# Optimization experiments

Measured on AMD Instinct MI355X. Metric: run time of the kernel, lower is better.

Reference implementation:

```python
import jax, jax.numpy as jnp
import numpy as np

D_MODEL = 1024
N_HEADS = 16
HEAD_DIM = D_MODEL // N_HEADS


def setup_inputs() -> dict:
    key = jax.random.key(0)
    ks = jax.random.split(key, 9)
    s = 1.0 / np.sqrt(D_MODEL)
    x = jax.random.normal(ks[0], (1, 4096, D_MODEL), dtype=jnp.float32)
    Wq = jax.random.uniform(ks[1], (D_MODEL, D_MODEL), jnp.float32, -s, s)
    bq = jax.random.uniform(ks[2], (D_MODEL,), jnp.float32, -s, s)
    Wk = jax.random.uniform(ks[3], (D_MODEL, D_MODEL), jnp.float32, -s, s)
    bk = jax.random.uniform(ks[4], (D_MODEL,), jnp.float32, -s, s)
    Wv = jax.random.uniform(ks[5], (D_MODEL, D_MODEL), jnp.float32, -s, s)
    bv = jax.random.uniform(ks[6], (D_MODEL,), jnp.float32, -s, s)
    Wo = jax.random.uniform(ks[7], (D_MODEL, D_MODEL), jnp.float32, -s, s)
    bo = jax.random.uniform(ks[8], (D_MODEL,), jnp.float32, -s, s)
    return {"x": x, "Wq": Wq, "bq": bq, "Wk": Wk, "bk": bk,
            "Wv": Wv, "bv": bv, "Wo": Wo, "bo": bo, "layer_id": 0}


def reference(x, Wq, bq, Wk, bk, Wv, bv, Wo, bo, layer_id):
    # Fresh-cache path: K/V projected from x, then cached (cache omitted here).
    B, T, C = x.shape
    H, Dh = N_HEADS, HEAD_DIM

    def proj(W, b):
        # nn.Linear: x @ W.T + b, then split heads -> [B, H, T, Dh]
        y = jnp.einsum('btc,dc->btd', x, W) + b
        return y.reshape(B, T, H, Dh).transpose(0, 2, 1, 3)

    q = proj(Wq, bq)
    k = proj(Wk, bk)
    v = proj(Wv, bv)

    scores = jnp.einsum('bhqd,bhkd->bhqk', q, k) * (Dh ** -0.5)
    attn = jax.nn.softmax(scores, axis=-1)
    out = jnp.einsum('bhqk,bhkd->bhqd', attn, v)  # [B,H,T,Dh]
    out = out.transpose(0, 2, 1, 3).reshape(B, T, C)
    return jnp.einsum('btc,dc->btd', out, Wo) + bo
```

## Files before the change

kernel.cpp:

```cpp
#include <hip/hip_runtime.h>
#include <stdint.h>
#include <math.h>

#define T_SEQ 4096
#define DM 1024
#define NH 16
#define DH 64
#define QSCALE 0.1803368801111137f

typedef unsigned short u16;
typedef __attribute__((ext_vector_type(8))) short bfx8;
typedef __attribute__((ext_vector_type(4))) float f4;
typedef __attribute__((ext_vector_type(16))) float f16f;
typedef __attribute__((ext_vector_type(4))) uint32_t u32x4;

__device__ inline u16 f2bf(float f) {
  uint32_t u = __float_as_uint(f);
  u = (u + 0x7fffu + ((u >> 16) & 1u)) >> 16;
  return (u16)u;
}

__device__ inline uint32_t cvtpk(float lo, float hi) {
  uint32_t r;
  asm("v_cvt_pk_bf16_f32 %0, %1, %2" : "=v"(r) : "v"(lo), "v"(hi));
  return r;
}
__device__ inline void pl32(uint32_t &a, uint32_t &b) {
  asm volatile("v_permlane32_swap_b32 %0, %1" : "+v"(a), "+v"(b));
}

__device__ inline void gl_lds16(const void* g, void* l) {
  __builtin_amdgcn_global_load_lds(
      (__attribute__((address_space(1))) uint32_t*)const_cast<void*>(g),
      (__attribute__((address_space(3))) uint32_t*)l, 16, 0, 0);
}

__global__ __launch_bounds__(256) void cvt_kernel(const float* __restrict__ src,
                                                  u16* __restrict__ dst, int n8) {
  int i = blockIdx.x * 256 + threadIdx.x;
  if (i >= n8) return;
  const float4* s = (const float4*)src + (size_t)i * 2;
  float4 a = s[0], b = s[1];
  union { u16 u[8]; bfx8 v; } o;
  o.u[0] = f2bf(a.x); o.u[1] = f2bf(a.y); o.u[2] = f2bf(a.z); o.u[3] = f2bf(a.w);
  o.u[4] = f2bf(b.x); o.u[5] = f2bf(b.y); o.u[6] = f2bf(b.z); o.u[7] = f2bf(b.w);
  *(bfx8*)(dst + (size_t)i * 8) = o.v;
}

__global__ __launch_bounds__(256) void cvt4_kernel(
    const float* __restrict__ a, const float* __restrict__ b,
    const float* __restrict__ c, const float* __restrict__ d,
    u16* __restrict__ oa, u16* __restrict__ ob, u16* __restrict__ oc, u16* __restrict__ od) {
  int z = blockIdx.y;
  const float* s = (z == 0) ? a : (z == 1) ? b : (z == 2) ? c : d;
  u16* o = (z == 0) ? oa : (z == 1) ? ob : (z == 2) ? oc : od;
  int i = blockIdx.x * 256 + threadIdx.x;
  const float4* sp = (const float4*)s + (size_t)i * 2;
  float4 x = sp[0], y = sp[1];
  union { u16 u[8]; bfx8 v; } t;
  t.u[0] = f2bf(x.x); t.u[1] = f2bf(x.y); t.u[2] = f2bf(x.z); t.u[3] = f2bf(x.w);
  t.u[4] = f2bf(y.x); t.u[5] = f2bf(y.y); t.u[6] = f2bf(y.z); t.u[7] = f2bf(y.w);
  *(bfx8*)(o + (size_t)i * 8) = t.v;
}

__global__ __launch_bounds__(256) void gemm_qkv(
    const u16* __restrict__ xb,
    const u16* __restrict__ wq, const u16* __restrict__ wk, const u16* __restrict__ wv,
    const float* __restrict__ bq, const float* __restrict__ bk, const float* __restrict__ bv,
    u16* __restrict__ qo, u16* __restrict__ ko, u16* __restrict__ vo) {
  __shared__ u16 sA[128 * 32];
  __shared__ u16 sB[128 * 32];
  const int mode = blockIdx.z;
  const u16* w = (mode == 0) ? wq : (mode == 1) ? wk : wv;
  const float* bias = (mode == 0) ? bq : (mode == 1) ? bk : bv;
  const int tid = threadIdx.x, lane = tid & 63, wid = tid >> 6;
  const int wr = wid >> 1, wc = wid & 1;
  const int row0 = blockIdx.y * 128, col0 = blockIdx.x * 128;
  f4 acc[4][4] = {};

  for (int kt = 0; kt < DM / 32; ++kt) {
#pragma unroll
    for (int i = 0; i < 2; ++i) {
      int c = i * 4 + wid;
      int r = c * 16 + (lane >> 2);
      int s = (lane & 3) ^ ((r >> 1) & 3);
      gl_lds16(xb + (size_t)(row0 + r) * DM + kt * 32 + s * 8, &sA[c * 512 + lane * 8]);
      gl_lds16(w  + (size_t)(col0 + r) * DM + kt * 32 + s * 8, &sB[c * 512 + lane * 8]);
    }
    __syncthreads();
    bfx8 a[4], b[4];
#pragma unroll
    for (int t = 0; t < 4; ++t) {
      int ra = wr * 64 + t * 16 + (lane & 15);
      a[t] = *(const bfx8*)&sA[ra * 32 + (((lane >> 4) ^ ((ra >> 1) & 3)) * 8)];
      int rb = wc * 64 + t * 16 + (lane & 15);
      b[t] = *(const bfx8*)&sB[rb * 32 + (((lane >> 4) ^ ((rb >> 1) & 3)) * 8)];
    }
#pragma unroll
    for (int mt = 0; mt < 4; ++mt)
#pragma unroll
      for (int nt = 0; nt < 4; ++nt)
        acc[mt][nt] = __builtin_amdgcn_mfma_f32_16x16x32_bf16(a[mt], b[nt], acc[mt][nt], 0, 0, 0);
    __syncthreads();
  }

#pragma unroll
  for (int mt = 0; mt < 4; ++mt) {
#pragma unroll
    for (int nt = 0; nt < 4; ++nt) {
      int n = col0 + wc * 64 + nt * 16 + (lane & 15);
      float bv_ = bias[n];
      int h = n >> 6, d = n & 63;
#pragma unroll
      for (int r = 0; r < 4; ++r) {
        int mrow = row0 + wr * 64 + mt * 16 + (lane >> 4) * 4 + r;
        float v = acc[mt][nt][r] + bv_;
        if (mode == 0)      qo[(size_t)h * (T_SEQ * DH) + (size_t)mrow * DH + d] = f2bf(v * QSCALE);
        else if (mode == 1) ko[(size_t)h * (T_SEQ * DH) + (size_t)mrow * DH + d] = f2bf(v);
        else                vo[(size_t)h * (DH * T_SEQ) + (size_t)d * T_SEQ + mrow] = f2bf(v);
      }
    }
  }
}

__global__ __launch_bounds__(256) void gemm_out(
    const u16* __restrict__ ab, const u16* __restrict__ wo,
    const float* __restrict__ bo, float* __restrict__ out) {
  __shared__ u16 sA[128 * 32];
  __shared__ u16 sB[128 * 32];
  const int tid = threadIdx.x, lane = tid & 63, wid = tid >> 6;
  const int wr = wid >> 1, wc = wid & 1;
  const int row0 = blockIdx.y * 128, col0 = blockIdx.x * 128;
  f4 acc[4][4] = {};

  for (int kt = 0; kt < DM / 32; ++kt) {
#pragma unroll
    for (int i = 0; i < 2; ++i) {
      int c = i * 4 + wid;
      int r = c * 16 + (lane >> 2);
      int s = (lane & 3) ^ ((r >> 1) & 3);
      gl_lds16(ab + (size_t)(row0 + r) * DM + kt * 32 + s * 8, &sA[c * 512 + lane * 8]);
      gl_lds16(wo + (size_t)(col0 + r) * DM + kt * 32 + s * 8, &sB[c * 512 + lane * 8]);
    }
    __syncthreads();
    bfx8 a[4], b[4];
#pragma unroll
    for (int t = 0; t < 4; ++t) {
      int ra = wr * 64 + t * 16 + (lane & 15);
      a[t] = *(const bfx8*)&sA[ra * 32 + (((lane >> 4) ^ ((ra >> 1) & 3)) * 8)];
      int rb = wc * 64 + t * 16 + (lane & 15);
      b[t] = *(const bfx8*)&sB[rb * 32 + (((lane >> 4) ^ ((rb >> 1) & 3)) * 8)];
    }
#pragma unroll
    for (int mt = 0; mt < 4; ++mt)
#pragma unroll
      for (int nt = 0; nt < 4; ++nt)
        acc[mt][nt] = __builtin_amdgcn_mfma_f32_16x16x32_bf16(a[mt], b[nt], acc[mt][nt], 0, 0, 0);
    __syncthreads();
  }

#pragma unroll
  for (int mt = 0; mt < 4; ++mt) {
#pragma unroll
    for (int nt = 0; nt < 4; ++nt) {
      int n = col0 + wc * 64 + nt * 16 + (lane & 15);
      float bv_ = bo[n];
#pragma unroll
      for (int r = 0; r < 4; ++r) {
        int mrow = row0 + wr * 64 + mt * 16 + (lane >> 4) * 4 + r;
        out[(size_t)mrow * DM + n] = acc[mt][nt][r] + bv_;
      }
    }
  }
}

__global__ __launch_bounds__(512, 2) void attn_kernel(
    const u16* __restrict__ qb, const u16* __restrict__ kb,
    const u16* __restrict__ vb, u16* __restrict__ ao) {
  __shared__ u16 sK[2][64 * 64];
  __shared__ u16 sV[2][64 * 64];
  const int tid = threadIdx.x, lane = tid & 63, wid = tid >> 6;
  const int hi = lane >> 5, q32 = lane & 31;
  const int bid = blockIdx.x;
  const int h = (bid & 7) * 2 + ((bid >> 3) & 1);
  const int qr0 = (bid >> 4) * 256 + wid * 32;
  const size_t hoff = (size_t)h * ((size_t)T_SEQ * DH);

  bfx8 qf0, qf1, qf2, qf3;
  {
    const u16* qp = qb + hoff + (size_t)(qr0 + q32) * DH + hi * 8;
    qf0 = *(const bfx8*)(qp);
    qf1 = *(const bfx8*)(qp + 16);
    qf2 = *(const bfx8*)(qp + 32);
    qf3 = *(const bfx8*)(qp + 48);
  }

  f16f o0 = {}, o1 = {};
  float m = -INFINITY, l = 0.f;

  const int sr = tid >> 3, ssl = (tid & 7) ^ (sr & 7);
  const u16* kg = kb + hoff + (size_t)sr * DH + ssl * 8;
  const u16* vg = vb + hoff + (size_t)sr * T_SEQ + ssl * 8;
  u16* dK0 = &sK[0][tid * 8]; u16* dK1 = &sK[1][tid * 8];
  u16* dV0 = &sV[0][tid * 8]; u16* dV1 = &sV[1][tid * 8];

  gl_lds16(kg, dK0);
  gl_lds16(vg, dV0);
  __syncthreads();

  const int NT = T_SEQ / 64;
  const int x0 = (q32 & 7) * 8;
  for (int kt = 0; kt < NT; ++kt) {
    const u16* Kc = (kt & 1) ? sK[1] : sK[0];
    const u16* Vc = (kt & 1) ? sV[1] : sV[0];
    if (kt + 1 < NT) {
      gl_lds16(kg + (size_t)(kt + 1) * 64 * DH, (kt & 1) ? dK0 : dK1);
      gl_lds16(vg + (size_t)(kt + 1) * 64,     (kt & 1) ? dV0 : dV1);
    }

    f16f s0 = {}, s1 = {};
    {
      const int c0 = q32 * 64, c1 = (32 + q32) * 64;
#define QKSTEP(ds, QF)                                                              \
      {                                                                             \
        bfx8 kf0 = *(const bfx8*)&Kc[c0 + (((2 * ds + hi) * 8) ^ x0)];              \
        s0 = __builtin_amdgcn_mfma_f32_32x32x16_bf16(kf0, QF, s0, 0, 0, 0);         \
        bfx8 kf1 = *(const bfx8*)&Kc[c1 + (((2 * ds + hi) * 8) ^ x0)];              \
        s1 = __builtin_amdgcn_mfma_f32_32x32x16_bf16(kf1, QF, s1, 0, 0, 0);         \
      }
      QKSTEP(0, qf0) QKSTEP(1, qf1) QKSTEP(2, qf2) QKSTEP(3, qf3)
#undef QKSTEP
    }

    float tm = fmaxf(s0[0], s1[0]);
#pragma unroll
    for (int r = 1; r < 16; ++r) tm = fmaxf(tm, fmaxf(s0[r], s1[r]));
    tm = fmaxf(tm, __shfl_xor(tm, 32));
    float mn = fmaxf(m, tm);
    float fsc = __builtin_amdgcn_exp2f(m - mn);
    m = mn;
    float ps = 0.f;
#pragma unroll
    for (int r = 0; r < 16; ++r) { s0[r] = __builtin_amdgcn_exp2f(s0[r] - mn); ps += s0[r]; }
#pragma unroll
    for (int r = 0; r < 16; ++r) { s1[r] = __builtin_amdgcn_exp2f(s1[r] - mn); ps += s1[r]; }
    ps += __shfl_xor(ps, 32);
    l = l * fsc + ps;
#pragma unroll
    for (int r = 0; r < 16; ++r) { o0[r] *= fsc; o1[r] *= fsc; }

    uint32_t a0, a1, a2, a3;
    bfx8 pa0, pa1, pa2, pa3;
#define PACK(SS, i0, PA)                                                     \
    a0 = cvtpk(SS[i0 + 0], SS[i0 + 1]); a1 = cvtpk(SS[i0 + 2], SS[i0 + 3]);  \
    a2 = cvtpk(SS[i0 + 4], SS[i0 + 5]); a3 = cvtpk(SS[i0 + 6], SS[i0 + 7]);  \
    pl32(a0, a2); pl32(a1, a3);                                              \
    { u32x4 t_; t_[0] = a0; t_[1] = a1; t_[2] = a2; t_[3] = a3;              \
      PA = __builtin_bit_cast(bfx8, t_); }
    PACK(s0, 0, pa0) PACK(s0, 8, pa1) PACK(s1, 0, pa2) PACK(s1, 8, pa3)
#undef PACK

    {
      const int d0 = q32 * 64, d1 = (32 + q32) * 64;
#define PVSTEP(ks, PA)                                                              \
      {                                                                             \
        bfx8 vf0 = *(const bfx8*)&Vc[d0 + (((2 * ks + hi) * 8) ^ x0)];              \
        o0 = __builtin_amdgcn_mfma_f32_32x32x16_bf16(vf0, PA, o0, 0, 0, 0);         \
        bfx8 vf1 = *(const bfx8*)&Vc[d1 + (((2 * ks + hi) * 8) ^ x0)];              \
        o1 = __builtin_amdgcn_mfma_f32_32x32x16_bf16(vf1, PA, o1, 0, 0, 0);         \
      }
      PVSTEP(0, pa0) PVSTEP(1, pa1) PVSTEP(2, pa2) PVSTEP(3, pa3)
#undef PVSTEP
    }
    __syncthreads();
  }

  float inv = 1.0f / l;
  u16* orow = ao + (size_t)(qr0 + q32) * DM + h * DH;
#pragma unroll
  for (int r = 0; r < 16; ++r) {
    int d0 = (r & 3) + 8 * (r >> 2) + 4 * hi;
    orow[d0]      = f2bf(o0[r] * inv);
    orow[32 + d0] = f2bf(o1[r] * inv);
  }
}

extern "C" void kernel_launch(void* const* d_in, const int* in_sizes, int n_in,
                              void* d_out, int out_size, void* d_ws, size_t ws_size,
                              hipStream_t stream) {
  const float* x  = (const float*)d_in[0];
  const float* Wq = (const float*)d_in[1];
  const float* bq = (const float*)d_in[2];
  const float* Wk = (const float*)d_in[3];
  const float* bk = (const float*)d_in[4];
  const float* Wv = (const float*)d_in[5];
  const float* bv = (const float*)d_in[6];
  const float* Wo = (const float*)d_in[7];
  const float* bo = (const float*)d_in[8];
  float* out = (float*)d_out;

  u16* ws  = (u16*)d_ws;
  u16* xb  = ws;
  u16* wqb = xb + (size_t)T_SEQ * DM;
  u16* wkb = wqb + (size_t)DM * DM;
  u16* wvb = wkb + (size_t)DM * DM;
  u16* wob = wvb + (size_t)DM * DM;
  u16* qbb = wob + (size_t)DM * DM;
  u16* kbb = qbb + (size_t)T_SEQ * DM;
  u16* vbb = kbb + (size_t)T_SEQ * DM;
  u16* abb = vbb + (size_t)T_SEQ * DM;

  cvt_kernel<<<(T_SEQ * DM / 8) / 256, 256, 0, stream>>>(x, xb, T_SEQ * DM / 8);
  cvt4_kernel<<<dim3((DM * DM / 8) / 256, 4), 256, 0, stream>>>(
      Wq, Wk, Wv, Wo, wqb, wkb, wvb, wob);

  gemm_qkv<<<dim3(DM / 128, T_SEQ / 128, 3), 256, 0, stream>>>(
      xb, wqb, wkb, wvb, bq, bk, bv, qbb, kbb, vbb);

  attn_kernel<<<256, 512, 0, stream>>>(qbb, kbb, vbb, abb);

  gemm_out<<<dim3(DM / 128, T_SEQ / 128), 256, 0, stream>>>(abb, wob, bo, out);
}
```

Before: 243.8 us.

## Load K/V fragments straight from global into registers, drop LDS staging in attention

The attention kernel stops staging K and V tiles through double-buffered shared memory with block-wide barriers. Each wave now loads its K/V MFMA fragments directly from global memory into registers, prefetching the next K tile with register ping-pong. Blocks shrink to 256 threads (4 waves) with twice as many blocks. The softmax is reorganized with tree reductions and a lazy rescale that only updates the running max when it grows by more than 8, and s_setprio is raised around the MFMA bursts. The cost is that every wave re-reads K/V from global or L2 instead of sharing them across the block, and the lazy max leaves exp values up to 2^8, which reduces precision headroom.

```diff
diff --git a/kernel.cpp b/kernel.cpp
--- a/kernel.cpp
+++ b/kernel.cpp
@@ -174,16 +174,59 @@
   }
 }
 
-__global__ __launch_bounds__(512, 2) void attn_kernel(
+
+#define MFMA32(A, B, C) __builtin_amdgcn_mfma_f32_32x32x16_bf16(A, B, C, 0, 0, 0)
+
+__device__ __forceinline__ void softmax_pack(
+    f16f& s0, f16f& s1, float& m, float& l, f16f& o0, f16f& o1,
+    bfx8& pa0, bfx8& pa1, bfx8& pa2, bfx8& pa3) {
+  float u[8];
+#pragma unroll
+  for (int r = 0; r < 8; ++r) u[r] = fmaxf(s0[r], s0[r + 8]);
+#pragma unroll
+  for (int r = 0; r < 8; ++r) u[r] = fmaxf(u[r], fmaxf(s1[r], s1[r + 8]));
+  float tm = fmaxf(fmaxf(fmaxf(u[0], u[1]), fmaxf(u[2], u[3])),
+                   fmaxf(fmaxf(u[4], u[5]), fmaxf(u[6], u[7])));
+  tm = fmaxf(tm, __shfl_xor(tm, 32));
+  if (!__all(tm <= m + 8.0f)) {
+    float mn = fmaxf(m, tm);
+    float fsc = __builtin_amdgcn_exp2f(m - mn);
+    m = mn; l *= fsc;
+#pragma unroll
+    for (int r = 0; r < 16; ++r) { o0[r] *= fsc; o1[r] *= fsc; }
+  }
+#pragma unroll
+  for (int r = 0; r < 16; ++r) s0[r] = __builtin_amdgcn_exp2f(s0[r] - m);
+#pragma unroll
+  for (int r = 0; r < 16; ++r) s1[r] = __builtin_amdgcn_exp2f(s1[r] - m);
+  float q0 = 0.f, q1 = 0.f, q2 = 0.f, q3 = 0.f;
+#pragma unroll
+  for (int r = 0; r < 4; ++r) {
+    q0 += s0[r]; q1 += s0[r + 4]; q2 += s0[r + 8]; q3 += s0[r + 12];
+    q0 += s1[r]; q1 += s1[r + 4]; q2 += s1[r + 8]; q3 += s1[r + 12];
+  }
+  float ps = (q0 + q1) + (q2 + q3);
+  ps += __shfl_xor(ps, 32);
+  l += ps;
+  uint32_t a0, a1, a2, a3;
+#define PACK(SS, i0, PA)                                                     \
+  a0 = cvtpk(SS[i0 + 0], SS[i0 + 1]); a1 = cvtpk(SS[i0 + 2], SS[i0 + 3]);    \
+  a2 = cvtpk(SS[i0 + 4], SS[i0 + 5]); a3 = cvtpk(SS[i0 + 6], SS[i0 + 7]);    \
+  pl32(a0, a2); pl32(a1, a3);                                                \
+  { u32x4 t_; t_[0] = a0; t_[1] = a1; t_[2] = a2; t_[3] = a3;                \
+    PA = __builtin_bit_cast(bfx8, t_); }
+  PACK(s0, 0, pa0) PACK(s0, 8, pa1) PACK(s1, 0, pa2) PACK(s1, 8, pa3)
+#undef PACK
+}
+
+__global__ __launch_bounds__(256, 2) void attn_kernel(
     const u16* __restrict__ qb, const u16* __restrict__ kb,
     const u16* __restrict__ vb, u16* __restrict__ ao) {
-  __shared__ u16 sK[2][64 * 64];
-  __shared__ u16 sV[2][64 * 64];
   const int tid = threadIdx.x, lane = tid & 63, wid = tid >> 6;
   const int hi = lane >> 5, q32 = lane & 31;
   const int bid = blockIdx.x;
   const int h = (bid & 7) * 2 + ((bid >> 3) & 1);
-  const int qr0 = (bid >> 4) * 256 + wid * 32;
+  const int qr0 = (bid >> 4) * 128 + wid * 32;
   const size_t hoff = (size_t)h * ((size_t)T_SEQ * DH);
 
   bfx8 qf0, qf1, qf2, qf3;
@@ -198,82 +241,59 @@
   f16f o0 = {}, o1 = {};
   float m = -INFINITY, l = 0.f;
 
-  const int sr = tid >> 3, ssl = (tid & 7) ^ (sr & 7);
-  const u16* kg = kb + hoff + (size_t)sr * DH + ssl * 8;
-  const u16* vg = vb + hoff + (size_t)sr * T_SEQ + ssl * 8;
-  u16* dK0 = &sK[0][tid * 8]; u16* dK1 = &sK[1][tid * 8];
-  u16* dV0 = &sV[0][tid * 8]; u16* dV1 = &sV[1][tid * 8];
-
-  gl_lds16(kg, dK0);
-  gl_lds16(vg, dV0);
-  __syncthreads();
+  const u16* kp0 = kb + hoff + (size_t)q32 * DH + hi * 8;
+  const u16* kp1 = kp0 + 32 * DH;
+  const u16* vp0 = vb + hoff + (size_t)q32 * T_SEQ + hi * 8;
+  const u16* vp1 = vp0 + (size_t)32 * T_SEQ;
+
+  bfx8 Aa0, Aa1, Aa2, Aa3, Ab0, Ab1, Ab2, Ab3;
+  bfx8 Ba0 = {}, Ba1 = {}, Ba2 = {}, Ba3 = {}, Bb0 = {}, Bb1 = {}, Bb2 = {}, Bb3 = {};
+
+  Aa0 = *(const bfx8*)(kp0);      Aa1 = *(const bfx8*)(kp0 + 16);
+  Aa2 = *(const bfx8*)(kp0 + 32); Aa3 = *(const bfx8*)(kp0 + 48);
+  Ab0 = *(const bfx8*)(kp1);      Ab1 = *(const bfx8*)(kp1 + 16);
+  Ab2 = *(const bfx8*)(kp1 + 32); Ab3 = *(const bfx8*)(kp1 + 48);
+  kp0 += 64 * DH; kp1 += 64 * DH;
 
   const int NT = T_SEQ / 64;
-  const int x0 = (q32 & 7) * 8;
-  for (int kt = 0; kt < NT; ++kt) {
-    const u16* Kc = (kt & 1) ? sK[1] : sK[0];
-    const u16* Vc = (kt & 1) ? sV[1] : sV[0];
-    if (kt + 1 < NT) {
-      gl_lds16(kg + (size_t)(kt + 1) * 64 * DH, (kt & 1) ? dK0 : dK1);
-      gl_lds16(vg + (size_t)(kt + 1) * 64,     (kt & 1) ? dV0 : dV1);
-    }
-
-    f16f s0 = {}, s1 = {};
-    {
-      const int c0 = q32 * 64, c1 = (32 + q32) * 64;
-#define QKSTEP(ds, QF)                                                              \
-      {                                                                             \
-        bfx8 kf0 = *(const bfx8*)&Kc[c0 + (((2 * ds + hi) * 8) ^ x0)];              \
-        s0 = __builtin_amdgcn_mfma_f32_32x32x16_bf16(kf0, QF, s0, 0, 0, 0);         \
-        bfx8 kf1 = *(const bfx8*)&Kc[c1 + (((2 * ds + hi) * 8) ^ x0)];              \
-        s1 = __builtin_amdgcn_mfma_f32_32x32x16_bf16(kf1, QF, s1, 0, 0, 0);         \
-      }
-      QKSTEP(0, qf0) QKSTEP(1, qf1) QKSTEP(2, qf2) QKSTEP(3, qf3)
-#undef QKSTEP
-    }
-
-    float tm = fmaxf(s0[0], s1[0]);
-#pragma unroll
-    for (int r = 1; r < 16; ++r) tm = fmaxf(tm, fmaxf(s0[r], s1[r]));
-    tm = fmaxf(tm, __shfl_xor(tm, 32));
-    float mn = fmaxf(m, tm);
-    float fsc = __builtin_amdgcn_exp2f(m - mn);
-    m = mn;
-    float ps = 0.f;
-#pragma unroll
-    for (int r = 0; r < 16; ++r) { s0[r] = __builtin_amdgcn_exp2f(s0[r] - mn); ps += s0[r]; }
-#pragma unroll
-    for (int r = 0; r < 16; ++r) { s1[r] = __builtin_amdgcn_exp2f(s1[r] - mn); ps += s1[r]; }
-    ps += __shfl_xor(ps, 32);
-    l = l * fsc + ps;
-#pragma unroll
-    for (int r = 0; r < 16; ++r) { o0[r] *= fsc; o1[r] *= fsc; }
-
-    uint32_t a0, a1, a2, a3;
-    bfx8 pa0, pa1, pa2, pa3;
-#define PACK(SS, i0, PA)                                                     \
-    a0 = cvtpk(SS[i0 + 0], SS[i0 + 1]); a1 = cvtpk(SS[i0 + 2], SS[i0 + 3]);  \
-    a2 = cvtpk(SS[i0 + 4], SS[i0 + 5]); a3 = cvtpk(SS[i0 + 6], SS[i0 + 7]);  \
-    pl32(a0, a2); pl32(a1, a3);                                              \
-    { u32x4 t_; t_[0] = a0; t_[1] = a1; t_[2] = a2; t_[3] = a3;              \
-      PA = __builtin_bit_cast(bfx8, t_); }
-    PACK(s0, 0, pa0) PACK(s0, 8, pa1) PACK(s1, 0, pa2) PACK(s1, 8, pa3)
-#undef PACK
-
-    {
-      const int d0 = q32 * 64, d1 = (32 + q32) * 64;
-#define PVSTEP(ks, PA)                                                              \
-      {                                                                             \
-        bfx8 vf0 = *(const bfx8*)&Vc[d0 + (((2 * ks + hi) * 8) ^ x0)];              \
-        o0 = __builtin_amdgcn_mfma_f32_32x32x16_bf16(vf0, PA, o0, 0, 0, 0);         \
-        bfx8 vf1 = *(const bfx8*)&Vc[d1 + (((2 * ks + hi) * 8) ^ x0)];              \
-        o1 = __builtin_amdgcn_mfma_f32_32x32x16_bf16(vf1, PA, o1, 0, 0, 0);         \
-      }
-      PVSTEP(0, pa0) PVSTEP(1, pa1) PVSTEP(2, pa2) PVSTEP(3, pa3)
-#undef PVSTEP
-    }
-    __syncthreads();
-  }
+
+#define PHASE(KC, KN, PREF)                                                    \
+  {                                                                            \
+             \
+    bfx8 w0 = *(const bfx8*)(vp0);       bfx8 w1 = *(const bfx8*)(vp0 + 16);   \
+    bfx8 w2 = *(const bfx8*)(vp0 + 32);  bfx8 w3 = *(const bfx8*)(vp0 + 48);   \
+    bfx8 y0 = *(const bfx8*)(vp1);       bfx8 y1 = *(const bfx8*)(vp1 + 16);   \
+    bfx8 y2 = *(const bfx8*)(vp1 + 32);  bfx8 y3 = *(const bfx8*)(vp1 + 48);   \
+    vp0 += 64; vp1 += 64;                                                      \
+    if (PREF) {                \
+      KN##a0 = *(const bfx8*)(kp0);      KN##a1 = *(const bfx8*)(kp0 + 16);    \
+      KN##a2 = *(const bfx8*)(kp0 + 32); KN##a3 = *(const bfx8*)(kp0 + 48);    \
+      KN##b0 = *(const bfx8*)(kp1);      KN##b1 = *(const bfx8*)(kp1 + 16);    \
+      KN##b2 = *(const bfx8*)(kp1 + 32); KN##b3 = *(const bfx8*)(kp1 + 48);    \
+      kp0 += 64 * DH; kp1 += 64 * DH;                                          \
+    }                                                                          \
+    f16f s0 = {}, s1 = {};                                                     \
+    __builtin_amdgcn_s_setprio(1);                                             \
+    s0 = MFMA32(KC##a0, qf0, s0); s1 = MFMA32(KC##b0, qf0, s1);                \
+    s0 = MFMA32(KC##a1, qf1, s0); s1 = MFMA32(KC##b1, qf1, s1);                \
+    s0 = MFMA32(KC##a2, qf2, s0); s1 = MFMA32(KC##b2, qf2, s1);                \
+    s0 = MFMA32(KC##a3, qf3, s0); s1 = MFMA32(KC##b3, qf3, s1);                \
+    __builtin_amdgcn_s_setprio(0);                                             \
+    bfx8 pa0, pa1, pa2, pa3;                                                   \
+    softmax_pack(s0, s1, m, l, o0, o1, pa0, pa1, pa2, pa3);                    \
+    __builtin_amdgcn_s_setprio(1);                                             \
+    o0 = MFMA32(w0, pa0, o0); o1 = MFMA32(y0, pa0, o1);                        \
+    o0 = MFMA32(w1, pa1, o0); o1 = MFMA32(y1, pa1, o1);                        \
+    o0 = MFMA32(w2, pa2, o0); o1 = MFMA32(y2, pa2, o1);                        \
+    o0 = MFMA32(w3, pa3, o0); o1 = MFMA32(y3, pa3, o1);                        \
+    __builtin_amdgcn_s_setprio(0);                                             \
+  }
+
+  for (int kt = 0; kt < NT; kt += 2) {
+    PHASE(A, B, true)
+    PHASE(B, A, (kt + 2 < NT))
+  }
+#undef PHASE
 
   float inv = 1.0f / l;
   u16* orow = ao + (size_t)(qr0 + q32) * DM + h * DH;
@@ -317,7 +337,7 @@
   gemm_qkv<<<dim3(DM / 128, T_SEQ / 128, 3), 256, 0, stream>>>(
       xb, wqb, wkb, wvb, bq, bk, bv, qbb, kbb, vbb);
 
-  attn_kernel<<<256, 512, 0, stream>>>(qbb, kbb, vbb, abb);
+  attn_kernel<<<512, 256, 0, stream>>>(qbb, kbb, vbb, abb);
 
   gemm_out<<<dim3(DM / 128, T_SEQ / 128), 256, 0, stream>>>(abb, wob, bo, out);
 }
```

Measured after the change: 379.2 us. +55.5%, slower.

## Split attention KV range in two blocks with merge kernel and lazy rescale

Applied to the files above, without the earlier changes.

Splits each attention query tile's KV sequence into two halves handled by separate blocks (512 blocks instead of 256), writing fp32 partial outputs plus max/sum stats that a new merge kernel combines into bf16. This targets the low occupancy of the original 256-block grid on a 256-CU device. The change also adds a lazy rescale that skips the o/l update when the max rises by less than 8, packed-float max/sum reductions, s_setprio around MFMA blocks, and raises launch bounds occupancy to 4. In exchange it adds fp32 partial-output traffic (about 32 MB written and read) and an extra kernel launch.

```diff
diff --git a/kernel.cpp b/kernel.cpp
--- a/kernel.cpp
+++ b/kernel.cpp
@@ -13,6 +13,7 @@
 typedef __attribute__((ext_vector_type(4))) float f4;
 typedef __attribute__((ext_vector_type(16))) float f16f;
 typedef __attribute__((ext_vector_type(4))) uint32_t u32x4;
+typedef __attribute__((ext_vector_type(2))) float f2;
 
 __device__ inline u16 f2bf(float f) {
   uint32_t u = __float_as_uint(f);
@@ -33,6 +34,11 @@
   __builtin_amdgcn_global_load_lds(
       (__attribute__((address_space(1))) uint32_t*)const_cast<void*>(g),
       (__attribute__((address_space(3))) uint32_t*)l, 16, 0, 0);
+}
+
+__device__ __forceinline__ f2 mkf2(float a, float b) { f2 r; r[0] = a; r[1] = b; return r; }
+__device__ __forceinline__ f2 pkmax(f2 a, f2 b) {
+  f2 r; r[0] = fmaxf(a[0], b[0]); r[1] = fmaxf(a[1], b[1]); return r;
 }
 
 __global__ __launch_bounds__(256) void cvt_kernel(const float* __restrict__ src,
@@ -174,16 +180,73 @@
   }
 }
 
-__global__ __launch_bounds__(512, 2) void attn_kernel(
+
+#define MFMA32(A, B, C) __builtin_amdgcn_mfma_f32_32x32x16_bf16(A, B, C, 0, 0, 0)
+
+__device__ __forceinline__ void softmax_pack(
+    f16f& s0, f16f& s1, float& m, float& l, f16f& o0, f16f& o1,
+    bfx8& pa0, bfx8& pa1, bfx8& pa2, bfx8& pa3) {
+  f2 a0 = pkmax(mkf2(s0[0], s0[1]),   mkf2(s0[2], s0[3]));
+  f2 a1 = pkmax(mkf2(s0[4], s0[5]),   mkf2(s0[6], s0[7]));
+  f2 a2 = pkmax(mkf2(s0[8], s0[9]),   mkf2(s0[10], s0[11]));
+  f2 a3 = pkmax(mkf2(s0[12], s0[13]), mkf2(s0[14], s0[15]));
+  f2 b0 = pkmax(mkf2(s1[0], s1[1]),   mkf2(s1[2], s1[3]));
+  f2 b1 = pkmax(mkf2(s1[4], s1[5]),   mkf2(s1[6], s1[7]));
+  f2 b2 = pkmax(mkf2(s1[8], s1[9]),   mkf2(s1[10], s1[11]));
+  f2 b3 = pkmax(mkf2(s1[12], s1[13]), mkf2(s1[14], s1[15]));
+  a0 = pkmax(a0, a1); a2 = pkmax(a2, a3);
+  b0 = pkmax(b0, b1); b2 = pkmax(b2, b3);
+  a0 = pkmax(pkmax(a0, a2), pkmax(b0, b2));
+  float tm = fmaxf(a0[0], a0[1]);
+  tm = fmaxf(tm, __shfl_xor(tm, 32));
+  if (!__all(tm <= m + 8.0f)) {
+    float mn = fmaxf(m, tm);
+    float fsc = __builtin_amdgcn_exp2f(m - mn);
+    m = mn; l *= fsc;
+#pragma unroll
+    for (int r = 0; r < 16; ++r) { o0[r] *= fsc; o1[r] *= fsc; }
+  }
+  f2 m2 = mkf2(m, m);
+#pragma unroll
+  for (int r = 0; r < 16; r += 2) {
+    f2 t = mkf2(s0[r], s0[r + 1]) - m2;
+    s0[r] = __builtin_amdgcn_exp2f(t[0]); s0[r + 1] = __builtin_amdgcn_exp2f(t[1]);
+  }
+#pragma unroll
+  for (int r = 0; r < 16; r += 2) {
+    f2 t = mkf2(s1[r], s1[r + 1]) - m2;
+    s1[r] = __builtin_amdgcn_exp2f(t[0]); s1[r + 1] = __builtin_amdgcn_exp2f(t[1]);
+  }
+  f2 c0 = (mkf2(s0[0], s0[1]) + mkf2(s0[2], s0[3])) + (mkf2(s0[4], s0[5]) + mkf2(s0[6], s0[7]));
+  f2 c1 = (mkf2(s0[8], s0[9]) + mkf2(s0[10], s0[11])) + (mkf2(s0[12], s0[13]) + mkf2(s0[14], s0[15]));
+  f2 c2 = (mkf2(s1[0], s1[1]) + mkf2(s1[2], s1[3])) + (mkf2(s1[4], s1[5]) + mkf2(s1[6], s1[7]));
+  f2 c3 = (mkf2(s1[8], s1[9]) + mkf2(s1[10], s1[11])) + (mkf2(s1[12], s1[13]) + mkf2(s1[14], s1[15]));
+  c0 = (c0 + c1) + (c2 + c3);
+  float ps = c0[0] + c0[1];
+  ps += __shfl_xor(ps, 32);
+  l += ps;
+  uint32_t x0, x1, x2, x3;
+#define PACK(SS, i0, PA)                                                     \
+  x0 = cvtpk(SS[i0 + 0], SS[i0 + 1]); x1 = cvtpk(SS[i0 + 2], SS[i0 + 3]);    \
+  x2 = cvtpk(SS[i0 + 4], SS[i0 + 5]); x3 = cvtpk(SS[i0 + 6], SS[i0 + 7]);    \
+  pl32(x0, x2); pl32(x1, x3);                                                \
+  { u32x4 t_; t_[0] = x0; t_[1] = x1; t_[2] = x2; t_[3] = x3;                \
+    PA = __builtin_bit_cast(bfx8, t_); }
+  PACK(s0, 0, pa0) PACK(s0, 8, pa1) PACK(s1, 0, pa2) PACK(s1, 8, pa3)
+#undef PACK
+}
+
+__global__ __launch_bounds__(512, 4) void attn_kernel(
     const u16* __restrict__ qb, const u16* __restrict__ kb,
-    const u16* __restrict__ vb, u16* __restrict__ ao) {
+    const u16* __restrict__ vb, float* __restrict__ opart, float* __restrict__ mlb) {
   __shared__ u16 sK[2][64 * 64];
   __shared__ u16 sV[2][64 * 64];
   const int tid = threadIdx.x, lane = tid & 63, wid = tid >> 6;
   const int hi = lane >> 5, q32 = lane & 31;
   const int bid = blockIdx.x;
   const int h = (bid & 7) * 2 + ((bid >> 3) & 1);
-  const int qr0 = (bid >> 4) * 256 + wid * 32;
+  const int half = (bid >> 4) & 1;
+  const int qr0 = (bid >> 5) * 256 + wid * 32;
   const size_t hoff = (size_t)h * ((size_t)T_SEQ * DH);
 
   bfx8 qf0, qf1, qf2, qf3;
@@ -199,8 +262,8 @@
   float m = -INFINITY, l = 0.f;
 
   const int sr = tid >> 3, ssl = (tid & 7) ^ (sr & 7);
-  const u16* kg = kb + hoff + (size_t)sr * DH + ssl * 8;
-  const u16* vg = vb + hoff + (size_t)sr * T_SEQ + ssl * 8;
+  const u16* kg = kb + hoff + (size_t)(half * 2048 + sr) * DH + ssl * 8;
+  const u16* vg = vb + hoff + (size_t)sr * T_SEQ + half * 2048 + ssl * 8;
   u16* dK0 = &sK[0][tid * 8]; u16* dK1 = &sK[1][tid * 8];
   u16* dV0 = &sV[0][tid * 8]; u16* dV1 = &sV[1][tid * 8];
 
@@ -208,12 +271,12 @@
   gl_lds16(vg, dV0);
   __syncthreads();
 
-  const int NT = T_SEQ / 64;
-  const int x0 = (q32 & 7) * 8;
-  for (int kt = 0; kt < NT; ++kt) {
+  const int NTH = 2048 / 64;
+  const int x0s = (q32 & 7) * 8;
+  for (int kt = 0; kt < NTH; ++kt) {
     const u16* Kc = (kt & 1) ? sK[1] : sK[0];
     const u16* Vc = (kt & 1) ? sV[1] : sV[0];
-    if (kt + 1 < NT) {
+    if (kt + 1 < NTH) {
       gl_lds16(kg + (size_t)(kt + 1) * 64 * DH, (kt & 1) ? dK0 : dK1);
       gl_lds16(vg + (size_t)(kt + 1) * 64,     (kt & 1) ? dV0 : dV1);
     }
@@ -221,68 +284,71 @@
     f16f s0 = {}, s1 = {};
     {
       const int c0 = q32 * 64, c1 = (32 + q32) * 64;
+      __builtin_amdgcn_s_setprio(1);
 #define QKSTEP(ds, QF)                                                              \
       {                                                                             \
-        bfx8 kf0 = *(const bfx8*)&Kc[c0 + (((2 * ds + hi) * 8) ^ x0)];              \
-        s0 = __builtin_amdgcn_mfma_f32_32x32x16_bf16(kf0, QF, s0, 0, 0, 0);         \
-        bfx8 kf1 = *(const bfx8*)&Kc[c1 + (((2 * ds + hi) * 8) ^ x0)];              \
-        s1 = __builtin_amdgcn_mfma_f32_32x32x16_bf16(kf1, QF, s1, 0, 0, 0);         \
+        bfx8 kf0 = *(const bfx8*)&Kc[c0 + (((2 * ds + hi) * 8) ^ x0s)];             \
+        s0 = MFMA32(kf0, QF, s0);                                                   \
+        bfx8 kf1 = *(const bfx8*)&Kc[c1 + (((2 * ds + hi) * 8) ^ x0s)];             \
+        s1 = MFMA32(kf1, QF, s1);                                                   \
       }
       QKSTEP(0, qf0) QKSTEP(1, qf1) QKSTEP(2, qf2) QKSTEP(3, qf3)
 #undef QKSTEP
-    }
-
-    float tm = fmaxf(s0[0], s1[0]);
-#pragma unroll
-    for (int r = 1; r < 16; ++r) tm = fmaxf(tm, fmaxf(s0[r], s1[r]));
-    tm = fmaxf(tm, __shfl_xor(tm, 32));
-    float mn = fmaxf(m, tm);
-    float fsc = __builtin_amdgcn_exp2f(m - mn);
-    m = mn;
-    float ps = 0.f;
-#pragma unroll
-    for (int r = 0; r < 16; ++r) { s0[r] = __builtin_amdgcn_exp2f(s0[r] - mn); ps += s0[r]; }
-#pragma unroll
-    for (int r = 0; r < 16; ++r) { s1[r] = __builtin_amdgcn_exp2f(s1[r] - mn); ps += s1[r]; }
-    ps += __shfl_xor(ps, 32);
-    l = l * fsc + ps;
-#pragma unroll
-    for (int r = 0; r < 16; ++r) { o0[r] *= fsc; o1[r] *= fsc; }
-
-    uint32_t a0, a1, a2, a3;
+      __builtin_amdgcn_s_setprio(0);
+    }
+
     bfx8 pa0, pa1, pa2, pa3;
-#define PACK(SS, i0, PA)                                                     \
-    a0 = cvtpk(SS[i0 + 0], SS[i0 + 1]); a1 = cvtpk(SS[i0 + 2], SS[i0 + 3]);  \
-    a2 = cvtpk(SS[i0 + 4], SS[i0 + 5]); a3 = cvtpk(SS[i0 + 6], SS[i0 + 7]);  \
-    pl32(a0, a2); pl32(a1, a3);                                              \
-    { u32x4 t_; t_[0] = a0; t_[1] = a1; t_[2] = a2; t_[3] = a3;              \
-      PA = __builtin_bit_cast(bfx8, t_); }
-    PACK(s0, 0, pa0) PACK(s0, 8, pa1) PACK(s1, 0, pa2) PACK(s1, 8, pa3)
-#undef PACK
+    softmax_pack(s0, s1, m, l, o0, o1, pa0, pa1, pa2, pa3);
 
     {
       const int d0 = q32 * 64, d1 = (32 + q32) * 64;
+      __builtin_amdgcn_s_setprio(1);
 #define PVSTEP(ks, PA)                                                              \
       {                                                                             \
-        bfx8 vf0 = *(const bfx8*)&Vc[d0 + (((2 * ks + hi) * 8) ^ x0)];              \
-        o0 = __builtin_amdgcn_mfma_f32_32x32x16_bf16(vf0, PA, o0, 0, 0, 0);         \
-        bfx8 vf1 = *(const bfx8*)&Vc[d1 + (((2 * ks + hi) * 8) ^ x0)];              \
-        o1 = __builtin_amdgcn_mfma_f32_32x32x16_bf16(vf1, PA, o1, 0, 0, 0);         \
+        bfx8 vf0 = *(const bfx8*)&Vc[d0 + (((2 * ks + hi) * 8) ^ x0s)];             \
+        o0 = MFMA32(vf0, PA, o0);                                                   \
+        bfx8 vf1 = *(const bfx8*)&Vc[d1 + (((2 * ks + hi) * 8) ^ x0s)];             \
+        o1 = MFMA32(vf1, PA, o1);                                                   \
       }
       PVSTEP(0, pa0) PVSTEP(1, pa1) PVSTEP(2, pa2) PVSTEP(3, pa3)
 #undef PVSTEP
-    }
-    __syncthreads();
-  }
-
-  float inv = 1.0f / l;
-  u16* orow = ao + (size_t)(qr0 + q32) * DM + h * DH;
-#pragma unroll
-  for (int r = 0; r < 16; ++r) {
-    int d0 = (r & 3) + 8 * (r >> 2) + 4 * hi;
-    orow[d0]      = f2bf(o0[r] * inv);
-    orow[32 + d0] = f2bf(o1[r] * inv);
-  }
+      __builtin_amdgcn_s_setprio(0);
+    }
+    __syncthreads();
+  }
+
+  const int R = h * T_SEQ + qr0 + q32;
+  float* op = opart + (size_t)half * (65536ull * 64) + (size_t)R * 64;
+#pragma unroll
+  for (int g = 0; g < 4; ++g) {
+    float4 t0; t0.x = o0[4 * g]; t0.y = o0[4 * g + 1]; t0.z = o0[4 * g + 2]; t0.w = o0[4 * g + 3];
+    *(float4*)(op + 8 * g + 4 * hi) = t0;
+    float4 t1; t1.x = o1[4 * g]; t1.y = o1[4 * g + 1]; t1.z = o1[4 * g + 2]; t1.w = o1[4 * g + 3];
+    *(float4*)(op + 32 + 8 * g + 4 * hi) = t1;
+  }
+  if (hi == 0) {
+    float2 t; t.x = m; t.y = l;
+    *(float2*)(mlb + (size_t)(half * 65536 + R) * 2) = t;
+  }
+}
+
+__global__ __launch_bounds__(256) void merge_kernel(
+    const float* __restrict__ op, const float* __restrict__ mlb,
+    u16* __restrict__ ao) {
+  const int tid = threadIdx.x;
+  const int lane = tid & 63;
+  const int rsub = tid >> 6;
+  const int R = blockIdx.x * 4 + rsub;
+  const int h = R >> 12, qrow = R & 4095;
+  const float m0 = mlb[(size_t)R * 2],             l0 = mlb[(size_t)R * 2 + 1];
+  const float m1 = mlb[(size_t)(65536 + R) * 2],   l1 = mlb[(size_t)(65536 + R) * 2 + 1];
+  float mm = fmaxf(m0, m1);
+  float f0 = __builtin_amdgcn_exp2f(m0 - mm);
+  float f1 = __builtin_amdgcn_exp2f(m1 - mm);
+  float inv = 1.0f / (f0 * l0 + f1 * l1);
+  float v0 = op[(size_t)R * 64 + lane];
+  float v1 = op[65536ull * 64 + (size_t)R * 64 + lane];
+  ao[(size_t)qrow * DM + h * DH + lane] = f2bf((f0 * v0 + f1 * v1) * inv);
 }
 
 extern "C" void kernel_launch(void* const* d_in, const int* in_sizes, int n_in,
@@ -309,6 +375,8 @@
   u16* kbb = qbb + (size_t)T_SEQ * DM;
   u16* vbb = kbb + (size_t)T_SEQ * DM;
   u16* abb = vbb + (size_t)T_SEQ * DM;
+  float* opart = (float*)(abb + (size_t)T_SEQ * DM);
+  float* mlb   = opart + 2ull * 65536 * 64;
 
   cvt_kernel<<<(T_SEQ * DM / 8) / 256, 256, 0, stream>>>(x, xb, T_SEQ * DM / 8);
   cvt4_kernel<<<dim3((DM * DM / 8) / 256, 4), 256, 0, stream>>>(
@@ -317,7 +385,8 @@
   gemm_qkv<<<dim3(DM / 128, T_SEQ / 128, 3), 256, 0, stream>>>(
       xb, wqb, wkb, wvb, bq, bk, bv, qbb, kbb, vbb);
 
-  attn_kernel<<<256, 512, 0, stream>>>(qbb, kbb, vbb, abb);
+  attn_kernel<<<512, 512, 0, stream>>>(qbb, kbb, vbb, opart, mlb);
+  merge_kernel<<<65536 / 4, 256, 0, stream>>>(opart, mlb, abb);
 
   gemm_out<<<dim3(DM / 128, T_SEQ / 128), 256, 0, stream>>>(abb, wob, bo, out);
 }
```

Result: no change. 246.6 us (+1.1%).
